# Performance work log

Measured on AMD Instinct MI355X. Metric: run time of the kernel, lower is better.

The kernel has to match this reference:

```python
import jax, jax.numpy as jnp
import numpy as np

DIM = 1024
NUM_HEADS = 16
HEAD_DIM = DIM // NUM_HEADS
ROPE_BASE = 10000.0


def rope_freqs(t):
    # [t, head_dim]: standard rotary angles, duplicated across both halves
    inv_freq = 1.0 / (ROPE_BASE ** (jnp.arange(0, HEAD_DIM, 2, dtype=jnp.float32) / HEAD_DIM))
    angles = jnp.arange(t, dtype=jnp.float32)[:, None] * inv_freq[None, :]  # [t, hd/2]
    return jnp.concatenate([angles, angles], axis=-1)  # [t, hd]


def rotate_half(x):
    x1, x2 = jnp.split(x, 2, axis=-1)
    return jnp.concatenate([-x2, x1], axis=-1)


def apply_rope(freqs, x):
    # freqs: [t, hd] broadcast to x: [b, h, t, hd]
    cos = jnp.cos(freqs)[None, None]
    sin = jnp.sin(freqs)[None, None]
    return x * cos + rotate_half(x) * sin


def setup_inputs() -> dict:
    key = jax.random.key(0)
    k1, k2, k3 = jax.random.split(key, 3)
    b, t = 2, 2048
    x = jax.random.normal(k1, (b, t, DIM), dtype=jnp.float32)
    Wqkv = jax.random.normal(k2, (DIM, 3 * DIM), dtype=jnp.float32) * (DIM ** -0.5)
    Wout = jax.random.normal(k3, (DIM, DIM), dtype=jnp.float32) * (DIM ** -0.5)
    bout = jnp.zeros((DIM,), dtype=jnp.float32)
    return {"x": x, "Wqkv": Wqkv, "Wout": Wout, "bout": bout}


def reference(x, Wqkv, Wout, bout):
    b, t, c = x.shape
    scale = HEAD_DIM ** -0.5
    qkv = x @ Wqkv  # [b, t, 3c]
    q, k, v = jnp.split(qkv, 3, axis=-1)
    def to_heads(a):
        return a.reshape(b, t, NUM_HEADS, HEAD_DIM).transpose(0, 2, 1, 3)  # [b,h,t,hd]
    q, k, v = to_heads(q), to_heads(k), to_heads(v)
    freqs = rope_freqs(t)
    q = apply_rope(freqs, q)
    k = apply_rope(freqs, k)
    attn = jnp.einsum('bhqd,bhkd->bhqk', q, k) * scale
    attn = jax.nn.softmax(attn, axis=-1)
    out = jnp.einsum('bhqk,bhkd->bhqd', attn, v)
    out = out.transpose(0, 2, 1, 3).reshape(b, t, c)
    return out @ Wout + bout
```

## Files before the change

### kernel.cpp

```cpp
#include <hip/hip_runtime.h>
#include <hip/hip_bf16.h>
#include <cstdint>

#define TT 2048
#define HD 64
#define NH 16
#define CDIM 1024
#define N3 3072
#define BT 4096
#define QSCALE 0.18033688011112042f

using bf16 = __hip_bfloat16;
typedef __attribute__((ext_vector_type(4))) float f32x4;
typedef __attribute__((ext_vector_type(8))) short short8;
typedef __attribute__((ext_vector_type(8))) __bf16 bf16x8v;

__device__ __forceinline__ short f2bbits(float f) {
  __hip_bfloat16 h = __float2bfloat16(f);
  return __builtin_bit_cast(short, h);
}

__device__ __forceinline__ f32x4 mfma_bf16(short8 a, short8 b, f32x4 c) {
  return __builtin_amdgcn_mfma_f32_16x16x32_bf16(
      __builtin_bit_cast(bf16x8v, a), __builtin_bit_cast(bf16x8v, b), c, 0, 0, 0);
}

__device__ __forceinline__ void gll16(const void* g, void* l) {
  __builtin_amdgcn_global_load_lds(
      (const __attribute__((address_space(1))) void*)g,
      (__attribute__((address_space(3))) void*)l, 16, 0, 0);
}

__device__ __forceinline__ float exp2_fast(float x) {
  float r;
  asm("v_exp_f32 %0, %1" : "=v"(r) : "v"(x));
  return r;
}

__device__ __forceinline__ uint32_t pkbf16(float lo, float hi) {
  uint32_t lw = (uint32_t)(uint16_t)f2bbits(lo);
  uint32_t hw = (uint32_t)(uint16_t)f2bbits(hi);
  return (hw << 16) | lw;
}


__global__ __launch_bounds__(256) void cvt_f32_to_bf16(const float* __restrict__ in,
                                                       bf16* __restrict__ out, int n) {
  int idx = (blockIdx.x * 256 + threadIdx.x) * 8;
  if (idx >= n) return;
  float4 a = *(const float4*)(in + idx);
  float4 b = *(const float4*)(in + idx + 4);
  short8 o;
  o[0] = f2bbits(a.x); o[1] = f2bbits(a.y); o[2] = f2bbits(a.z); o[3] = f2bbits(a.w);
  o[4] = f2bbits(b.x); o[5] = f2bbits(b.y); o[6] = f2bbits(b.z); o[7] = f2bbits(b.w);
  *(short8*)(out + idx) = o;
}

__global__ __launch_bounds__(256) void transpose_to_bf16(const float* __restrict__ in,
                                                         bf16* __restrict__ out,
                                                         int R, int C) {
  __shared__ float tile[32][33];
  int c0 = blockIdx.x * 32, r0 = blockIdx.y * 32;
  int tx = threadIdx.x, ty = threadIdx.y;
#pragma unroll
  for (int i = 0; i < 32; i += 8)
    tile[ty + i][tx] = in[(size_t)(r0 + ty + i) * C + c0 + tx];
  __syncthreads();
#pragma unroll
  for (int i = 0; i < 32; i += 8)
    out[(size_t)(c0 + ty + i) * R + r0 + tx] = __float2bfloat16(tile[tx][ty + i]);
}

__global__ __launch_bounds__(256) void rope_table(float* __restrict__ cost,
                                                  float* __restrict__ sint) {
  int idx = blockIdx.x * 256 + threadIdx.x;
  int t = idx >> 5, i = idx & 31;
  double inv = exp(-(double)i / 32.0 * log(10000.0));
  double a = (double)t * inv;
  cost[idx] = (float)cos(a);
  sint[idx] = (float)sin(a);
}

__global__ __launch_bounds__(256) void transpose_v(const bf16* __restrict__ V,
                                                   bf16* __restrict__ VT) {
  __shared__ bf16 tile[32][33];
  int bh = blockIdx.z;
  int t0 = blockIdx.x * 32, d0 = blockIdx.y * 32;
  const bf16* src = V + (size_t)bh * TT * HD;
  bf16* dst = VT + (size_t)bh * TT * HD;
  int tx = threadIdx.x, ty = threadIdx.y;
#pragma unroll
  for (int i = 0; i < 32; i += 8)
    tile[ty + i][tx] = src[(size_t)(t0 + ty + i) * HD + d0 + tx];
  __syncthreads();
#pragma unroll
  for (int i = 0; i < 32; i += 8)
    dst[(size_t)(d0 + ty + i) * TT + t0 + tx] = tile[tx][ty + i];
}


__device__ __forceinline__ void gemm_core(const bf16* __restrict__ A, const bf16* __restrict__ Bt,
                                          int K, int m0, int n0, f32x4 acc[4][4],
                                          bf16* As, bf16* Bs) {
  int tid = threadIdx.x;
  int w = tid >> 6, l = tid & 63;
  int wm = (w >> 1) * 64, wn = (w & 1) * 64;
  for (int kt = 0; kt < K; kt += 64) {
#pragma unroll
    for (int it = 0; it < 4; ++it) {
      int ci = it * 256 + tid;
      int r = ci >> 3, cc = ci & 7;
      int sc = cc ^ (r & 7);
      gll16(A + (size_t)(m0 + r) * K + kt + sc * 8, As + (it * 256 + w * 64) * 8);
      gll16(Bt + (size_t)(n0 + r) * K + kt + sc * 8, Bs + (it * 256 + w * 64) * 8);
    }
    __syncthreads();
#pragma unroll
    for (int c = 0; c < 2; ++c) {
      short8 af[4], bfr[4];
#pragma unroll
      for (int i = 0; i < 4; ++i) {
        int row = wm + i * 16 + (l & 15);
        int colE = c * 32 + (l >> 4) * 8;
        af[i] = *(const short8*)(As + row * 64 + (colE ^ ((row & 7) << 3)));
      }
#pragma unroll
      for (int j = 0; j < 4; ++j) {
        int row = wn + j * 16 + (l & 15);
        int colE = c * 32 + (l >> 4) * 8;
        bfr[j] = *(const short8*)(Bs + row * 64 + (colE ^ ((row & 7) << 3)));
      }
#pragma unroll
      for (int i = 0; i < 4; ++i)
#pragma unroll
        for (int j = 0; j < 4; ++j)
          acc[i][j] = mfma_bf16(af[i], bfr[j], acc[i][j]);
    }
    __syncthreads();
  }
}

__global__ __launch_bounds__(256) void qkv_gemm(const bf16* __restrict__ xb,
                                                const bf16* __restrict__ WqkvT,
                                                const float* __restrict__ cost,
                                                const float* __restrict__ sint,
                                                bf16* __restrict__ Qb, bf16* __restrict__ Kb,
                                                bf16* __restrict__ Vb) {
  __shared__ bf16 As[128 * 64];
  __shared__ bf16 Bs[128 * 64];
  int m0 = blockIdx.y * 128, n0 = blockIdx.x * 128;
  f32x4 acc[4][4] = {};
  gemm_core(xb, WqkvT, CDIM, m0, n0, acc, As, Bs);
  int tid = threadIdx.x, w = tid >> 6, l = tid & 63;
  int wm = (w >> 1) * 64, wn = (w & 1) * 64;
  int which = n0 >> 10;
  int h = ((n0 + wn) & 1023) >> 6;
  bf16* Out = which == 0 ? Qb : (which == 1 ? Kb : Vb);
  if (which < 2) {
    float sc = (which == 0) ? QSCALE : 1.0f;
#pragma unroll
    for (int i = 0; i < 4; ++i)
#pragma unroll
      for (int r = 0; r < 4; ++r) {
        int m = m0 + wm + i * 16 + (l >> 4) * 4 + r;
        int b = m >> 11, t = m & 2047;
        size_t base = (((size_t)(b * NH + h)) * TT + t) * HD;
#pragma unroll
        for (int j = 0; j < 2; ++j) {
          int ii = j * 16 + (l & 15);
          float c = cost[t * 32 + ii], s = sint[t * 32 + ii];
          float x1 = acc[i][j][r], x2 = acc[i][j + 2][r];
          Out[base + ii]      = __float2bfloat16((x1 * c - x2 * s) * sc);
          Out[base + ii + 32] = __float2bfloat16((x2 * c + x1 * s) * sc);
        }
      }
  } else {
#pragma unroll
    for (int i = 0; i < 4; ++i)
#pragma unroll
      for (int r = 0; r < 4; ++r) {
        int m = m0 + wm + i * 16 + (l >> 4) * 4 + r;
        int b = m >> 11, t = m & 2047;
        size_t base = (((size_t)(b * NH + h)) * TT + t) * HD;
#pragma unroll
        for (int j = 0; j < 4; ++j)
          Out[base + ((j * 16 + (l & 15)))] = __float2bfloat16(acc[i][j][r]);
      }
  }
}

__global__ __launch_bounds__(256) void out_gemm(const bf16* __restrict__ Ob,
                                                const bf16* __restrict__ WoutT,
                                                const float* __restrict__ bout,
                                                float* __restrict__ out) {
  __shared__ bf16 As[128 * 64];
  __shared__ bf16 Bs[128 * 64];
  int m0 = blockIdx.y * 128, n0 = blockIdx.x * 128;
  f32x4 acc[4][4] = {};
  gemm_core(Ob, WoutT, CDIM, m0, n0, acc, As, Bs);
  int tid = threadIdx.x, w = tid >> 6, l = tid & 63;
  int wm = (w >> 1) * 64, wn = (w & 1) * 64;
#pragma unroll
  for (int i = 0; i < 4; ++i)
#pragma unroll
    for (int j = 0; j < 4; ++j)
#pragma unroll
      for (int r = 0; r < 4; ++r) {
        int m = m0 + wm + i * 16 + (l >> 4) * 4 + r;
        int n = n0 + wn + j * 16 + (l & 15);
        out[(size_t)m * CDIM + n] = acc[i][j][r] + bout[n];
      }
}

#define VP 68
__global__ __launch_bounds__(256) void attn(const bf16* __restrict__ Q,
                                            const bf16* __restrict__ K,
                                            const bf16* __restrict__ VT,
                                            bf16* __restrict__ O) {
  __shared__ bf16 Ks[64 * 64];
  __shared__ bf16 Vs[64 * VP];
  int bh = blockIdx.y, q0 = blockIdx.x * 64;
  int tid = threadIdx.x, w = tid >> 6, l = tid & 63;
  int g = l >> 4, qi = l & 15;

  const bf16* Qg = Q + ((size_t)bh * TT + q0) * HD;
  const bf16* Kg = K + (size_t)bh * TT * HD;
  const bf16* Vg = VT + (size_t)bh * TT * HD;

#pragma unroll
  for (int it = 0; it < 2; ++it) {
    int ci = it * 256 + tid, r = ci >> 3, cc = ci & 7;
    gll16(Qg + (size_t)r * HD + (cc ^ (r & 7)) * 8, &Ks[0] + (it * 256 + w * 64) * 8);
  }
  __syncthreads();
  short8 aq[2];
#pragma unroll
  for (int c = 0; c < 2; ++c) {
    int row = w * 16 + qi;
    int colE = c * 32 + g * 8;
    aq[c] = *(const short8*)(&Ks[row * 64 + (colE ^ ((row & 7) << 3))]);
  }
  __syncthreads();

  f32x4 oacc[4] = {};
  float lsum = 0.f;

  for (int kt = 0; kt < TT; kt += 64) {
    uint4 vreg[2];
#pragma unroll
    for (int it = 0; it < 2; ++it) {
      int ci = it * 256 + tid, r = ci >> 3, cc = ci & 7;
      gll16(Kg + (size_t)(kt + r) * HD + (cc ^ (r & 7)) * 8, &Ks[0] + (it * 256 + w * 64) * 8);
      vreg[it] = *(const uint4*)(Vg + (size_t)r * TT + kt + cc * 8);
    }
#pragma unroll
    for (int it = 0; it < 2; ++it) {
      int ci = it * 256 + tid, r = ci >> 3, cc = ci & 7;
      *(uint4*)(&Vs[r * VP + cc * 8]) = vreg[it];
    }
    __syncthreads();

    f32x4 s[4] = {};
#pragma unroll
    for (int kn = 0; kn < 4; ++kn) {
#pragma unroll
      for (int c = 0; c < 2; ++c) {
        int row = kn * 16 + qi;
        int colE = c * 32 + g * 8;
        short8 kf = *(const short8*)(&Ks[row * 64 + (colE ^ ((row & 7) << 3))]);
        s[kn] = mfma_bf16(kf, aq[c], s[kn]);
      }
    }

    uint32_t wlo[4], whi[4];
#pragma unroll
    for (int kn = 0; kn < 4; ++kn) {
      float p0 = exp2_fast(s[kn][0]);
      float p1 = exp2_fast(s[kn][1]);
      float p2 = exp2_fast(s[kn][2]);
      float p3 = exp2_fast(s[kn][3]);
      lsum += (p0 + p1) + (p2 + p3);
      wlo[kn] = pkbf16(p0, p1);
      whi[kn] = pkbf16(p2, p3);
    }

#pragma unroll
    for (int c = 0; c < 2; ++c) {
      union { short8 s8; uint32_t u[4]; } pa;
      pa.u[0] = wlo[2 * c];     pa.u[1] = whi[2 * c];
      pa.u[2] = wlo[2 * c + 1]; pa.u[3] = whi[2 * c + 1];
#pragma unroll
      for (int dn = 0; dn < 4; ++dn) {
        int row = dn * 16 + qi;
        int e1 = c * 32 + g * 4;
        uint2 v0 = *(const uint2*)(&Vs[row * VP + e1]);
        uint2 v1 = *(const uint2*)(&Vs[row * VP + e1 + 16]);
        union { short8 s8; uint32_t u[4]; } vb;
        vb.u[0] = v0.x; vb.u[1] = v0.y; vb.u[2] = v1.x; vb.u[3] = v1.y;
        oacc[dn] = mfma_bf16(pa.s8, vb.s8, oacc[dn]);
      }
    }
    __syncthreads();
  }

  float tot = lsum;
  tot += __shfl_xor(tot, 16, 64);
  tot += __shfl_xor(tot, 32, 64);

  int b = bh >> 4, hh = bh & 15;
#pragma unroll
  for (int r = 0; r < 4; ++r) {
    float lq = __shfl(tot, g * 4 + r, 64);
    float inv = 1.0f / lq;
    int t = q0 + w * 16 + g * 4 + r;
    bf16* Orow = O + ((size_t)(b * TT + t)) * CDIM + hh * HD;
#pragma unroll
    for (int dn = 0; dn < 4; ++dn)
      Orow[dn * 16 + qi] = __float2bfloat16(oacc[dn][r] * inv);
  }
}


extern "C" void kernel_launch(void* const* d_in, const int* in_sizes, int n_in,
                              void* d_out, int out_size, void* d_ws, size_t ws_size,
                              hipStream_t stream) {
  const float* x    = (const float*)d_in[0];
  const float* Wqkv = (const float*)d_in[1];
  const float* Wout = (const float*)d_in[2];
  const float* bout = (const float*)d_in[3];
  float* out = (float*)d_out;

  char* ws = (char*)d_ws;
  bf16* xb     = (bf16*)(ws);
  bf16* WqkvT  = (bf16*)(ws + 8388608);
  bf16* WoutT  = (bf16*)(ws + 14680064);
  bf16* Qb     = (bf16*)(ws + 16777216);
  bf16* Kb     = (bf16*)(ws + 25165824);
  bf16* Vb     = (bf16*)(ws + 33554432);
  bf16* VTb    = (bf16*)(ws + 41943040);
  float* cost  = (float*)(ws + 50331648);
  float* sint  = (float*)(ws + 50593792);
  bf16* Ob     = xb;

  cvt_f32_to_bf16<<<2048, 256, 0, stream>>>(x, xb, BT * CDIM);
  transpose_to_bf16<<<dim3(96, 32), dim3(32, 8), 0, stream>>>(Wqkv, WqkvT, CDIM, N3);
  transpose_to_bf16<<<dim3(32, 32), dim3(32, 8), 0, stream>>>(Wout, WoutT, CDIM, CDIM);
  rope_table<<<256, 256, 0, stream>>>(cost, sint);
  qkv_gemm<<<dim3(24, 32), 256, 0, stream>>>(xb, WqkvT, cost, sint, Qb, Kb, Vb);
  transpose_v<<<dim3(64, 2, 32), dim3(32, 8), 0, stream>>>(Vb, VTb);
  attn<<<dim3(32, 32), 256, 0, stream>>>(Qb, Kb, VTb, Ob);
  out_gemm<<<dim3(8, 32), 256, 0, stream>>>(Ob, WoutT, bout, out);
}
```

Baseline: 147.3 us.

## Process 128 queries per attention block, two 16-row tiles per wave

Each attention block now handles 128 query rows instead of 64, so each wave computes two 16-row query tiles against every K/V tile loaded into shared memory. This halves the K/V global loads and LDS staging per query and lets the loaded K fragments feed twice as many MFMAs. The cost is twice the accumulator registers per wave and half as many blocks (512 instead of 1024), which lowers occupancy and parallelism across the GPU's compute units.

```diff
diff --git a/kernel.cpp b/kernel.cpp
--- a/kernel.cpp
+++ b/kernel.cpp
@@ -219,7 +219,7 @@
                                             bf16* __restrict__ O) {
   __shared__ bf16 Ks[64 * 64];
   __shared__ bf16 Vs[64 * VP];
-  int bh = blockIdx.y, q0 = blockIdx.x * 64;
+  int bh = blockIdx.y, q0 = blockIdx.x * 128;
   int tid = threadIdx.x, w = tid >> 6, l = tid & 63;
   int g = l >> 4, qi = l & 15;
 
@@ -227,23 +227,32 @@
   const bf16* Kg = K + (size_t)bh * TT * HD;
   const bf16* Vg = VT + (size_t)bh * TT * HD;
 
-#pragma unroll
-  for (int it = 0; it < 2; ++it) {
-    int ci = it * 256 + tid, r = ci >> 3, cc = ci & 7;
-    gll16(Qg + (size_t)r * HD + (cc ^ (r & 7)) * 8, &Ks[0] + (it * 256 + w * 64) * 8);
-  }
-  __syncthreads();
-  short8 aq[2];
-#pragma unroll
-  for (int c = 0; c < 2; ++c) {
-    int row = w * 16 + qi;
-    int colE = c * 32 + g * 8;
-    aq[c] = *(const short8*)(&Ks[row * 64 + (colE ^ ((row & 7) << 3))]);
-  }
-  __syncthreads();
-
-  f32x4 oacc[4] = {};
-  float lsum = 0.f;
+  short8 aq[2][2];
+#pragma unroll
+  for (int pass = 0; pass < 2; ++pass) {
+#pragma unroll
+    for (int it = 0; it < 2; ++it) {
+      int ci = it * 256 + tid, r = ci >> 3, cc = ci & 7;
+      gll16(Qg + (size_t)(pass * 64 + r) * HD + (cc ^ (r & 7)) * 8,
+            &Ks[0] + (it * 256 + w * 64) * 8);
+    }
+    __syncthreads();
+    if ((w >> 1) == pass) {
+      int wl = w & 1;
+#pragma unroll
+      for (int m = 0; m < 2; ++m)
+#pragma unroll
+        for (int c = 0; c < 2; ++c) {
+          int row = wl * 32 + m * 16 + qi;
+          int colE = c * 32 + g * 8;
+          aq[m][c] = *(const short8*)(&Ks[row * 64 + (colE ^ ((row & 7) << 3))]);
+        }
+    }
+    __syncthreads();
+  }
+
+  f32x4 oacc[2][4] = {};
+  float lsum[2] = {0.f, 0.f};
 
   for (int kt = 0; kt < TT; kt += 64) {
     uint4 vreg[2];
@@ -260,35 +269,46 @@
     }
     __syncthreads();
 
-    f32x4 s[4] = {};
-#pragma unroll
-    for (int kn = 0; kn < 4; ++kn) {
+    short8 kf[4][2];
+#pragma unroll
+    for (int kn = 0; kn < 4; ++kn)
 #pragma unroll
       for (int c = 0; c < 2; ++c) {
         int row = kn * 16 + qi;
         int colE = c * 32 + g * 8;
-        short8 kf = *(const short8*)(&Ks[row * 64 + (colE ^ ((row & 7) << 3))]);
-        s[kn] = mfma_bf16(kf, aq[c], s[kn]);
-      }
-    }
-
-    uint32_t wlo[4], whi[4];
-#pragma unroll
-    for (int kn = 0; kn < 4; ++kn) {
-      float p0 = exp2_fast(s[kn][0]);
-      float p1 = exp2_fast(s[kn][1]);
-      float p2 = exp2_fast(s[kn][2]);
-      float p3 = exp2_fast(s[kn][3]);
-      lsum += (p0 + p1) + (p2 + p3);
-      wlo[kn] = pkbf16(p0, p1);
-      whi[kn] = pkbf16(p2, p3);
-    }
+        kf[kn][c] = *(const short8*)(&Ks[row * 64 + (colE ^ ((row & 7) << 3))]);
+      }
+    f32x4 s[2][4] = {};
+#pragma unroll
+    for (int m = 0; m < 2; ++m)
+#pragma unroll
+      for (int kn = 0; kn < 4; ++kn)
+#pragma unroll
+        for (int c = 0; c < 2; ++c)
+          s[m][kn] = mfma_bf16(kf[kn][c], aq[m][c], s[m][kn]);
+
+    uint32_t wlo[2][4], whi[2][4];
+#pragma unroll
+    for (int m = 0; m < 2; ++m)
+#pragma unroll
+      for (int kn = 0; kn < 4; ++kn) {
+        float p0 = exp2_fast(s[m][kn][0]);
+        float p1 = exp2_fast(s[m][kn][1]);
+        float p2 = exp2_fast(s[m][kn][2]);
+        float p3 = exp2_fast(s[m][kn][3]);
+        lsum[m] += (p0 + p1) + (p2 + p3);
+        wlo[m][kn] = pkbf16(p0, p1);
+        whi[m][kn] = pkbf16(p2, p3);
+      }
 
 #pragma unroll
     for (int c = 0; c < 2; ++c) {
-      union { short8 s8; uint32_t u[4]; } pa;
-      pa.u[0] = wlo[2 * c];     pa.u[1] = whi[2 * c];
-      pa.u[2] = wlo[2 * c + 1]; pa.u[3] = whi[2 * c + 1];
+      union { short8 s8; uint32_t u[4]; } pa[2];
+#pragma unroll
+      for (int m = 0; m < 2; ++m) {
+        pa[m].u[0] = wlo[m][2 * c];     pa[m].u[1] = whi[m][2 * c];
+        pa[m].u[2] = wlo[m][2 * c + 1]; pa[m].u[3] = whi[m][2 * c + 1];
+      }
 #pragma unroll
       for (int dn = 0; dn < 4; ++dn) {
         int row = dn * 16 + qi;
@@ -297,27 +317,36 @@
         uint2 v1 = *(const uint2*)(&Vs[row * VP + e1 + 16]);
         union { short8 s8; uint32_t u[4]; } vb;
         vb.u[0] = v0.x; vb.u[1] = v0.y; vb.u[2] = v1.x; vb.u[3] = v1.y;
-        oacc[dn] = mfma_bf16(pa.s8, vb.s8, oacc[dn]);
-      }
-    }
-    __syncthreads();
-  }
-
-  float tot = lsum;
-  tot += __shfl_xor(tot, 16, 64);
-  tot += __shfl_xor(tot, 32, 64);
+#pragma unroll
+        for (int m = 0; m < 2; ++m)
+          oacc[m][dn] = mfma_bf16(pa[m].s8, vb.s8, oacc[m][dn]);
+      }
+    }
+    __syncthreads();
+  }
+
+  float tot[2];
+#pragma unroll
+  for (int m = 0; m < 2; ++m) {
+    float t = lsum[m];
+    t += __shfl_xor(t, 16, 64);
+    t += __shfl_xor(t, 32, 64);
+    tot[m] = t;
+  }
 
   int b = bh >> 4, hh = bh & 15;
 #pragma unroll
-  for (int r = 0; r < 4; ++r) {
-    float lq = __shfl(tot, g * 4 + r, 64);
-    float inv = 1.0f / lq;
-    int t = q0 + w * 16 + g * 4 + r;
-    bf16* Orow = O + ((size_t)(b * TT + t)) * CDIM + hh * HD;
-#pragma unroll
-    for (int dn = 0; dn < 4; ++dn)
-      Orow[dn * 16 + qi] = __float2bfloat16(oacc[dn][r] * inv);
-  }
+  for (int m = 0; m < 2; ++m)
+#pragma unroll
+    for (int r = 0; r < 4; ++r) {
+      float lq = __shfl(tot[m], g * 4 + r, 64);
+      float inv = 1.0f / lq;
+      int t = q0 + w * 32 + m * 16 + g * 4 + r;
+      bf16* Orow = O + ((size_t)(b * TT + t)) * CDIM + hh * HD;
+#pragma unroll
+      for (int dn = 0; dn < 4; ++dn)
+        Orow[dn * 16 + qi] = __float2bfloat16(oacc[m][dn][r] * inv);
+    }
 }
 
 
@@ -348,6 +377,6 @@
   rope_table<<<256, 256, 0, stream>>>(cost, sint);
   qkv_gemm<<<dim3(24, 32), 256, 0, stream>>>(xb, WqkvT, cost, sint, Qb, Kb, Vb);
   transpose_v<<<dim3(64, 2, 32), dim3(32, 8), 0, stream>>>(Vb, VTb);
-  attn<<<dim3(32, 32), 256, 0, stream>>>(Qb, Kb, VTb, Ob);
+  attn<<<dim3(16, 32), 256, 0, stream>>>(Qb, Kb, VTb, Ob);
   out_gemm<<<dim3(8, 32), 256, 0, stream>>>(Ob, WoutT, bout, out);
 }
```

After: 151.2 us. 2.7% more time.

## Double-buffer K/V tiles in attention kernel to overlap loads with compute

Applied to the files above, without the earlier changes.

Adds a second LDS buffer for K and V tiles and prefetches the next tile before computing on the current one. The first tile is loaded ahead of the loop, and the next V tile is kept in registers and written to LDS after the PV MFMAs. This cuts one barrier per iteration and is meant to hide global load latency behind the QK and PV matrix work. In exchange it doubles LDS usage and adds register pressure, which may lower occupancy.

```diff
diff --git a/kernel.cpp b/kernel.cpp
--- a/kernel.cpp
+++ b/kernel.cpp
@@ -217,8 +217,8 @@
                                             const bf16* __restrict__ K,
                                             const bf16* __restrict__ VT,
                                             bf16* __restrict__ O) {
-  __shared__ bf16 Ks[64 * 64];
-  __shared__ bf16 Vs[64 * VP];
+  __shared__ bf16 Ks[2][64 * 64];
+  __shared__ bf16 Vs[2][64 * VP];
   int bh = blockIdx.y, q0 = blockIdx.x * 64;
   int tid = threadIdx.x, w = tid >> 6, l = tid & 63;
   int g = l >> 4, qi = l & 15;
@@ -230,7 +230,7 @@
 #pragma unroll
   for (int it = 0; it < 2; ++it) {
     int ci = it * 256 + tid, r = ci >> 3, cc = ci & 7;
-    gll16(Qg + (size_t)r * HD + (cc ^ (r & 7)) * 8, &Ks[0] + (it * 256 + w * 64) * 8);
+    gll16(Qg + (size_t)r * HD + (cc ^ (r & 7)) * 8, &Ks[0][0] + (it * 256 + w * 64) * 8);
   }
   __syncthreads();
   short8 aq[2];
@@ -238,7 +238,23 @@
   for (int c = 0; c < 2; ++c) {
     int row = w * 16 + qi;
     int colE = c * 32 + g * 8;
-    aq[c] = *(const short8*)(&Ks[row * 64 + (colE ^ ((row & 7) << 3))]);
+    aq[c] = *(const short8*)(&Ks[0][row * 64 + (colE ^ ((row & 7) << 3))]);
+  }
+  __syncthreads();
+
+  {
+    uint4 vreg[2];
+#pragma unroll
+    for (int it = 0; it < 2; ++it) {
+      int ci = it * 256 + tid, r = ci >> 3, cc = ci & 7;
+      gll16(Kg + (size_t)r * HD + (cc ^ (r & 7)) * 8, &Ks[0][0] + (it * 256 + w * 64) * 8);
+      vreg[it] = *(const uint4*)(Vg + (size_t)r * TT + cc * 8);
+    }
+#pragma unroll
+    for (int it = 0; it < 2; ++it) {
+      int ci = it * 256 + tid, r = ci >> 3, cc = ci & 7;
+      *(uint4*)(&Vs[0][r * VP + cc * 8]) = vreg[it];
+    }
   }
   __syncthreads();
 
@@ -246,19 +262,19 @@
   float lsum = 0.f;
 
   for (int kt = 0; kt < TT; kt += 64) {
-    uint4 vreg[2];
-#pragma unroll
-    for (int it = 0; it < 2; ++it) {
-      int ci = it * 256 + tid, r = ci >> 3, cc = ci & 7;
-      gll16(Kg + (size_t)(kt + r) * HD + (cc ^ (r & 7)) * 8, &Ks[0] + (it * 256 + w * 64) * 8);
-      vreg[it] = *(const uint4*)(Vg + (size_t)r * TT + kt + cc * 8);
-    }
-#pragma unroll
-    for (int it = 0; it < 2; ++it) {
-      int ci = it * 256 + tid, r = ci >> 3, cc = ci & 7;
-      *(uint4*)(&Vs[r * VP + cc * 8]) = vreg[it];
-    }
-    __syncthreads();
+    int cur = (kt >> 6) & 1, nb = cur ^ 1;
+    bool more = (kt + 64 < TT);
+
+    uint4 vnext[2];
+    if (more) {
+#pragma unroll
+      for (int it = 0; it < 2; ++it) {
+        int ci = it * 256 + tid, r = ci >> 3, cc = ci & 7;
+        gll16(Kg + (size_t)(kt + 64 + r) * HD + (cc ^ (r & 7)) * 8,
+              &Ks[nb][0] + (it * 256 + w * 64) * 8);
+        vnext[it] = *(const uint4*)(Vg + (size_t)r * TT + (kt + 64) + cc * 8);
+      }
+    }
 
     f32x4 s[4] = {};
 #pragma unroll
@@ -267,7 +283,7 @@
       for (int c = 0; c < 2; ++c) {
         int row = kn * 16 + qi;
         int colE = c * 32 + g * 8;
-        short8 kf = *(const short8*)(&Ks[row * 64 + (colE ^ ((row & 7) << 3))]);
+        short8 kf = *(const short8*)(&Ks[cur][row * 64 + (colE ^ ((row & 7) << 3))]);
         s[kn] = mfma_bf16(kf, aq[c], s[kn]);
       }
     }
@@ -293,11 +309,19 @@
       for (int dn = 0; dn < 4; ++dn) {
         int row = dn * 16 + qi;
         int e1 = c * 32 + g * 4;
-        uint2 v0 = *(const uint2*)(&Vs[row * VP + e1]);
-        uint2 v1 = *(const uint2*)(&Vs[row * VP + e1 + 16]);
+        uint2 v0 = *(const uint2*)(&Vs[cur][row * VP + e1]);
+        uint2 v1 = *(const uint2*)(&Vs[cur][row * VP + e1 + 16]);
         union { short8 s8; uint32_t u[4]; } vb;
         vb.u[0] = v0.x; vb.u[1] = v0.y; vb.u[2] = v1.x; vb.u[3] = v1.y;
         oacc[dn] = mfma_bf16(pa.s8, vb.s8, oacc[dn]);
+      }
+    }
+
+    if (more) {
+#pragma unroll
+      for (int it = 0; it < 2; ++it) {
+        int ci = it * 256 + tid, r = ci >> 3, cc = ci & 7;
+        *(uint4*)(&Vs[nb][r * VP + cc * 8]) = vnext[it];
       }
     }
     __syncthreads();
```

New measurement: 172.6 us. 1.17x slower.

## Fuse V transpose into QKV GEMM epilogue and raise MFMA priority in attention

Applied to the files above, without the earlier changes.

The QKV GEMM epilogue for V tiles now stages the accumulator transposed in shared memory and writes V^T directly with 16-byte stores. This removes the separate transpose_v kernel along with its global round trip and launch. Separately, the attention kernel wraps its MFMA sections in s_setprio(1)/s_setprio(0) to favour matrix work over other waves. The fused epilogue adds extra barriers and reuses the GEMM's shared buffers, and only blocks that produce V take this path.

```diff
diff --git a/kernel.cpp b/kernel.cpp
--- a/kernel.cpp
+++ b/kernel.cpp
@@ -81,23 +81,6 @@
   sint[idx] = (float)sin(a);
 }
 
-__global__ __launch_bounds__(256) void transpose_v(const bf16* __restrict__ V,
-                                                   bf16* __restrict__ VT) {
-  __shared__ bf16 tile[32][33];
-  int bh = blockIdx.z;
-  int t0 = blockIdx.x * 32, d0 = blockIdx.y * 32;
-  const bf16* src = V + (size_t)bh * TT * HD;
-  bf16* dst = VT + (size_t)bh * TT * HD;
-  int tx = threadIdx.x, ty = threadIdx.y;
-#pragma unroll
-  for (int i = 0; i < 32; i += 8)
-    tile[ty + i][tx] = src[(size_t)(t0 + ty + i) * HD + d0 + tx];
-  __syncthreads();
-#pragma unroll
-  for (int i = 0; i < 32; i += 8)
-    dst[(size_t)(d0 + ty + i) * TT + t0 + tx] = tile[tx][ty + i];
-}
-
 
 __device__ __forceinline__ void gemm_core(const bf16* __restrict__ A, const bf16* __restrict__ Bt,
                                           int K, int m0, int n0, f32x4 acc[4][4],
@@ -145,18 +128,19 @@
                                                 const float* __restrict__ cost,
                                                 const float* __restrict__ sint,
                                                 bf16* __restrict__ Qb, bf16* __restrict__ Kb,
-                                                bf16* __restrict__ Vb) {
-  __shared__ bf16 As[128 * 64];
-  __shared__ bf16 Bs[128 * 64];
+                                                bf16* __restrict__ VTb) {
+  __shared__ bf16 Sh[2 * 128 * 64];
+  bf16* As = Sh;
+  bf16* Bs = Sh + 128 * 64;
   int m0 = blockIdx.y * 128, n0 = blockIdx.x * 128;
   f32x4 acc[4][4] = {};
   gemm_core(xb, WqkvT, CDIM, m0, n0, acc, As, Bs);
   int tid = threadIdx.x, w = tid >> 6, l = tid & 63;
   int wm = (w >> 1) * 64, wn = (w & 1) * 64;
   int which = n0 >> 10;
-  int h = ((n0 + wn) & 1023) >> 6;
-  bf16* Out = which == 0 ? Qb : (which == 1 ? Kb : Vb);
   if (which < 2) {
+    int h = ((n0 + wn) & 1023) >> 6;
+    bf16* Out = which == 0 ? Qb : Kb;
     float sc = (which == 0) ? QSCALE : 1.0f;
 #pragma unroll
     for (int i = 0; i < 4; ++i)
@@ -175,17 +159,34 @@
         }
       }
   } else {
-#pragma unroll
-    for (int i = 0; i < 4; ++i)
-#pragma unroll
-      for (int r = 0; r < 4; ++r) {
-        int m = m0 + wm + i * 16 + (l >> 4) * 4 + r;
-        int b = m >> 11, t = m & 2047;
-        size_t base = (((size_t)(b * NH + h)) * TT + t) * HD;
-#pragma unroll
-        for (int j = 0; j < 4; ++j)
-          Out[base + ((j * 16 + (l & 15)))] = __float2bfloat16(acc[i][j][r]);
-      }
+    const int BP = 136;
+    int hb = (n0 & 1023) >> 6;
+    int b = m0 >> 11, t0 = m0 & 2047;
+#pragma unroll
+    for (int p = 0; p < 2; ++p) {
+      if ((w & 1) == p) {
+#pragma unroll
+        for (int i = 0; i < 4; ++i)
+#pragma unroll
+          for (int j = 0; j < 4; ++j)
+#pragma unroll
+            for (int r = 0; r < 4; ++r) {
+              int dloc = j * 16 + (l & 15);
+              int mloc = wm + i * 16 + (l >> 4) * 4 + r;
+              Sh[dloc * BP + mloc] = __float2bfloat16(acc[i][j][r]);
+            }
+      }
+      __syncthreads();
+      {
+        int dloc = tid >> 2, tch = (tid & 3) * 32;
+        bf16* dst = VTb + (((size_t)(b * NH + hb + p)) * HD + dloc) * TT + t0 + tch;
+        const bf16* srcb = Sh + dloc * BP + tch;
+#pragma unroll
+        for (int k2 = 0; k2 < 4; ++k2)
+          *(uint4*)(dst + k2 * 8) = *(const uint4*)(srcb + k2 * 8);
+      }
+      __syncthreads();
+    }
   }
 }
 
@@ -261,6 +262,7 @@
     __syncthreads();
 
     f32x4 s[4] = {};
+    __builtin_amdgcn_s_setprio(1);
 #pragma unroll
     for (int kn = 0; kn < 4; ++kn) {
 #pragma unroll
@@ -271,6 +273,7 @@
         s[kn] = mfma_bf16(kf, aq[c], s[kn]);
       }
     }
+    __builtin_amdgcn_s_setprio(0);
 
     uint32_t wlo[4], whi[4];
 #pragma unroll
@@ -284,6 +287,7 @@
       whi[kn] = pkbf16(p2, p3);
     }
 
+    __builtin_amdgcn_s_setprio(1);
 #pragma unroll
     for (int c = 0; c < 2; ++c) {
       union { short8 s8; uint32_t u[4]; } pa;
@@ -300,6 +304,7 @@
         oacc[dn] = mfma_bf16(pa.s8, vb.s8, oacc[dn]);
       }
     }
+    __builtin_amdgcn_s_setprio(0);
     __syncthreads();
   }
 
@@ -336,7 +341,6 @@
   bf16* WoutT  = (bf16*)(ws + 14680064);
   bf16* Qb     = (bf16*)(ws + 16777216);
   bf16* Kb     = (bf16*)(ws + 25165824);
-  bf16* Vb     = (bf16*)(ws + 33554432);
   bf16* VTb    = (bf16*)(ws + 41943040);
   float* cost  = (float*)(ws + 50331648);
   float* sint  = (float*)(ws + 50593792);
@@ -346,8 +350,7 @@
   transpose_to_bf16<<<dim3(96, 32), dim3(32, 8), 0, stream>>>(Wqkv, WqkvT, CDIM, N3);
   transpose_to_bf16<<<dim3(32, 32), dim3(32, 8), 0, stream>>>(Wout, WoutT, CDIM, CDIM);
   rope_table<<<256, 256, 0, stream>>>(cost, sint);
-  qkv_gemm<<<dim3(24, 32), 256, 0, stream>>>(xb, WqkvT, cost, sint, Qb, Kb, Vb);
-  transpose_v<<<dim3(64, 2, 32), dim3(32, 8), 0, stream>>>(Vb, VTb);
+  qkv_gemm<<<dim3(24, 32), 256, 0, stream>>>(xb, WqkvT, cost, sint, Qb, Kb, VTb);
   attn<<<dim3(32, 32), 256, 0, stream>>>(Qb, Kb, VTb, Ob);
   out_gemm<<<dim3(8, 32), 256, 0, stream>>>(Ob, WoutT, bout, out);
 }
```

New measurement: 140.3 us. -4.7%, faster.
